# Optimization experiments

Measured on AMD Instinct MI355X. Metric: run time of the kernel, lower is better.

The kernel has to match this reference:

```python
import jax, jax.numpy as jnp
import numpy as np

B, T, I, H = 256, 2048, 64, 256


def setup_inputs() -> dict:
    key = jax.random.key(0)
    ks = jax.random.split(key, 8)
    s_ih = 1.0 / np.sqrt(H)
    return {
        "x": jax.random.normal(ks[0], (B, T, I), dtype=jnp.float32),
        "lengths": jax.random.randint(ks[1], (B,), 1, T + 1),  # in [1, T]
        "W_ih": jax.random.uniform(ks[2], (H, I), minval=-s_ih, maxval=s_ih),
        "W_hh": jax.random.uniform(ks[3], (H, H), minval=-s_ih, maxval=s_ih),
        "b_ih": jax.random.uniform(ks[4], (H,), minval=-s_ih, maxval=s_ih),
        "b_hh": jax.random.uniform(ks[5], (H,), minval=-s_ih, maxval=s_ih),
        "W_fc": jax.random.uniform(ks[6], (1, H), minval=-s_ih, maxval=s_ih),
        "b_fc": jax.random.uniform(ks[7], (1,), minval=-s_ih, maxval=s_ih),
    }


def reference(x, lengths, W_ih, W_hh, b_ih, b_hh, W_fc, b_fc):
    # Vanilla RNN (tanh), batch_first: h_t = tanh(x_t W_ih^T + b_ih + h_{t-1} W_hh^T + b_hh)
    batch = x.shape[0]
    h0 = jnp.zeros((batch, W_hh.shape[0]), dtype=x.dtype)
    # Precompute input projections for all timesteps in one big GEMM: [B, T, H]
    xp = jnp.einsum("bti,hi->bth", x, W_ih) + b_ih + b_hh

    def step(h, xt):  # xt: [B, H]
        h = jnp.tanh(xt + h @ W_hh.T)
        return h, h

    _, hs = jax.lax.scan(step, h0, jnp.swapaxes(xp, 0, 1))  # hs: [T, B, H]
    out = jnp.swapaxes(hs, 0, 1)  # [B, T, H]
    # Per-sample last valid timestep gather
    last = out[jnp.arange(batch), lengths - 1]  # [B, H]
    return last @ W_fc.T + b_fc  # [B, 1]
```

## Files before the change

kernel.cpp:

```cpp
#include <hip/hip_runtime.h>


static constexpr int nB = 256;
static constexpr int nT = 2048;
static constexpr int nI = 64;
static constexpr int nH = 256;
static constexpr int XBLK = 32;
static constexpr int THREADS = 512;

typedef _Float16 f16x8 __attribute__((ext_vector_type(8)));
typedef float f32x4 __attribute__((ext_vector_type(4)));

__device__ __forceinline__ float fast_tanh(float x) {
  float a = fabsf(x);
  float e = __expf(-2.0f * a);
  float r = (1.0f - e) / (1.0f + e);
  return copysignf(r, x);
}

__global__ __launch_bounds__(THREADS, 2)
void rnn_mfma(const float* __restrict__ x, const int* __restrict__ lengths,
              const float* __restrict__ Wih, const float* __restrict__ Whh,
              const float* __restrict__ bih, const float* __restrict__ bhh,
              const float* __restrict__ Wfc, const float* __restrict__ bfc,
              float* __restrict__ out)
{
  __shared__ __align__(16) _Float16 hbuf[2][nH];
  __shared__ __align__(16) _Float16 xbuf[2][XBLK * nI];
  __shared__ float red[THREADS / 64];

  const int b   = blockIdx.x;
  const int tid = threadIdx.x;
  const int w   = tid >> 6;
  const int l   = tid & 63;
  const int q   = l >> 4;
  const int n   = l & 15;
  const int len = lengths[b];
  const float* xb = x + (size_t)b * nT * nI;

  f16x8 Ah[2][8];
  f16x8 Ax[2][2];
#pragma unroll
  for (int mt = 0; mt < 2; ++mt) {
    const int row = 32 * w + 16 * mt + n;
#pragma unroll
    for (int kt = 0; kt < 8; ++kt) {
      const float* src = Whh + row * nH + 32 * kt + 8 * q;
      f16x8 a;
#pragma unroll
      for (int j = 0; j < 8; ++j) a[j] = (_Float16)src[j];
      Ah[mt][kt] = a;
    }
#pragma unroll
    for (int kt = 0; kt < 2; ++kt) {
      const float* src = Wih + row * nI + 32 * kt + 8 * q;
      f16x8 a;
#pragma unroll
      for (int j = 0; j < 8; ++j) a[j] = (_Float16)src[j];
      Ax[mt][kt] = a;
    }
  }
  f32x4 bias0, bias1;
#pragma unroll
  for (int r = 0; r < 4; ++r) {
    const int r0 = 32 * w + 4 * q + r;
    bias0[r] = bih[r0] + bhh[r0];
    bias1[r] = bih[r0 + 16] + bhh[r0 + 16];
  }
  const int mt_sel  = (n >> 2) & 1;
  const int reg_sel = n & 3;
  const int row_own = 32 * w + 16 * mt_sel + 4 * q + reg_sel;

  if (tid < nH) hbuf[0][tid] = (_Float16)0.f;
  {
    float4 v = *(const float4*)(xb + tid * 4);
    _Float16* d = xbuf[0] + tid * 4;
    d[0] = (_Float16)v.x; d[1] = (_Float16)v.y;
    d[2] = (_Float16)v.z; d[3] = (_Float16)v.w;
  }
  __syncthreads();

  int t = 0;
  for (int blk = 0; t < len; ++blk) {
    float4 pre;
    const bool havepre = ((blk + 1) * XBLK < len);
    if (havepre)
      pre = *(const float4*)(xb + (size_t)(blk + 1) * XBLK * nI + tid * 4);

    const int nsteps = min(XBLK, len - blk * XBLK);
    const _Float16* xB = xbuf[blk & 1];

    for (int s = 0; s < nsteps; ++s, ++t) {
      const _Float16* hsrc = hbuf[t & 1];
      const _Float16* xsrc = xB + s * nI;

      f32x4 acc0 = bias0, acc1 = bias1;
#pragma unroll
      for (int kt = 0; kt < 8; ++kt) {
        f16x8 Bh = *(const f16x8*)(hsrc + 32 * kt + 8 * q);
        acc0 = __builtin_amdgcn_mfma_f32_16x16x32_f16(Ah[0][kt], Bh, acc0, 0, 0, 0);
        acc1 = __builtin_amdgcn_mfma_f32_16x16x32_f16(Ah[1][kt], Bh, acc1, 0, 0, 0);
      }
#pragma unroll
      for (int kt = 0; kt < 2; ++kt) {
        f16x8 Bx = *(const f16x8*)(xsrc + 32 * kt + 8 * q);
        acc0 = __builtin_amdgcn_mfma_f32_16x16x32_f16(Ax[0][kt], Bx, acc0, 0, 0, 0);
        acc1 = __builtin_amdgcn_mfma_f32_16x16x32_f16(Ax[1][kt], Bx, acc1, 0, 0, 0);
      }

      f32x4 a = mt_sel ? acc1 : acc0;
      float lo = (reg_sel & 1) ? a[1] : a[0];
      float hi = (reg_sel & 1) ? a[3] : a[2];
      float v  = (reg_sel & 2) ? hi : lo;
      float hn = fast_tanh(v);

      if (s == nsteps - 1 && havepre) {
        _Float16* d = xbuf[(blk + 1) & 1] + tid * 4;
        d[0] = (_Float16)pre.x; d[1] = (_Float16)pre.y;
        d[2] = (_Float16)pre.z; d[3] = (_Float16)pre.w;
      }
      if (n < 8) hbuf[(t + 1) & 1][row_own] = (_Float16)hn;
      __syncthreads();
    }
  }

  float v = 0.f;
  if (tid < nH) v = (float)hbuf[len & 1][tid] * Wfc[tid];
#pragma unroll
  for (int off = 32; off; off >>= 1) v += __shfl_down(v, off);
  if (l == 0) red[w] = v;
  __syncthreads();
  if (tid == 0) {
    float acc = bfc[0];
#pragma unroll
    for (int i = 0; i < THREADS / 64; ++i) acc += red[i];
    out[b] = acc;
  }
}

extern "C" void kernel_launch(void* const* d_in, const int* in_sizes, int n_in,
                              void* d_out, int out_size, void* d_ws, size_t ws_size,
                              hipStream_t stream) {
  const float* x   = (const float*)d_in[0];
  const int* lens  = (const int*)d_in[1];
  const float* Wih = (const float*)d_in[2];
  const float* Whh = (const float*)d_in[3];
  const float* bih = (const float*)d_in[4];
  const float* bhh = (const float*)d_in[5];
  const float* Wfc = (const float*)d_in[6];
  const float* bfc = (const float*)d_in[7];
  float* out = (float*)d_out;

  rnn_mfma<<<nB, THREADS, 0, stream>>>(x, lens, Wih, Whh, bih, bhh, Wfc, bfc, out);
}
```

Before: 1.218 ms.

## Halve block to four waves, each computing four 16-row MFMA tiles per step

Cuts the block from 8 to 4 wavefronts, so each wave holds 64 rows of W_hh/W_ih in registers and issues four independent MFMA accumulation chains per step. This is meant to lower the cost of the per-timestep __syncthreads barrier and give each wave more independent MFMA work to hide latency. Every lane now writes one h element, and the x prefetch uses 8-wide f16 vector stores. In exchange, register pressure roughly doubles and the serial MFMA chain per wave gets longer, which may lengthen each step's critical path.

```diff
diff --git a/kernel.cpp b/kernel.cpp
--- a/kernel.cpp
+++ b/kernel.cpp
@@ -6,7 +6,7 @@
 static constexpr int nI = 64;
 static constexpr int nH = 256;
 static constexpr int XBLK = 32;
-static constexpr int THREADS = 512;
+static constexpr int THREADS = 256;
 
 typedef _Float16 f16x8 __attribute__((ext_vector_type(8)));
 typedef float f32x4 __attribute__((ext_vector_type(4)));
@@ -18,16 +18,16 @@
   return copysignf(r, x);
 }
 
-__global__ __launch_bounds__(THREADS, 2)
-void rnn_mfma(const float* __restrict__ x, const int* __restrict__ lengths,
-              const float* __restrict__ Wih, const float* __restrict__ Whh,
-              const float* __restrict__ bih, const float* __restrict__ bhh,
-              const float* __restrict__ Wfc, const float* __restrict__ bfc,
-              float* __restrict__ out)
+__global__ __launch_bounds__(THREADS, 1)
+void rnn_mfma4(const float* __restrict__ x, const int* __restrict__ lengths,
+               const float* __restrict__ Wih, const float* __restrict__ Whh,
+               const float* __restrict__ bih, const float* __restrict__ bhh,
+               const float* __restrict__ Wfc, const float* __restrict__ bfc,
+               float* __restrict__ out)
 {
   __shared__ __align__(16) _Float16 hbuf[2][nH];
   __shared__ __align__(16) _Float16 xbuf[2][XBLK * nI];
-  __shared__ float red[THREADS / 64];
+  __shared__ float red[4];
 
   const int b   = blockIdx.x;
   const int tid = threadIdx.x;
@@ -38,11 +38,11 @@
   const int len = lengths[b];
   const float* xb = x + (size_t)b * nT * nI;
 
-  f16x8 Ah[2][8];
-  f16x8 Ax[2][2];
+  f16x8 Ah[4][8];
+  f16x8 Ax[4][2];
 #pragma unroll
-  for (int mt = 0; mt < 2; ++mt) {
-    const int row = 32 * w + 16 * mt + n;
+  for (int mt = 0; mt < 4; ++mt) {
+    const int row = 64 * w + 16 * mt + n;
 #pragma unroll
     for (int kt = 0; kt < 8; ++kt) {
       const float* src = Whh + row * nH + 32 * kt + 8 * q;
@@ -60,32 +60,37 @@
       Ax[mt][kt] = a;
     }
   }
-  f32x4 bias0, bias1;
+  f32x4 bias[4];
 #pragma unroll
-  for (int r = 0; r < 4; ++r) {
-    const int r0 = 32 * w + 4 * q + r;
-    bias0[r] = bih[r0] + bhh[r0];
-    bias1[r] = bih[r0 + 16] + bhh[r0 + 16];
-  }
-  const int mt_sel  = (n >> 2) & 1;
+  for (int mt = 0; mt < 4; ++mt)
+#pragma unroll
+    for (int r = 0; r < 4; ++r) {
+      const int r0 = 64 * w + 16 * mt + 4 * q + r;
+      bias[mt][r] = bih[r0] + bhh[r0];
+    }
+  const int mt_sel  = n >> 2;
   const int reg_sel = n & 3;
-  const int row_own = 32 * w + 16 * mt_sel + 4 * q + reg_sel;
+  const int row_own = 64 * w + 16 * mt_sel + 4 * q + reg_sel;
 
-  if (tid < nH) hbuf[0][tid] = (_Float16)0.f;
+  hbuf[0][tid] = (_Float16)0.f;
   {
-    float4 v = *(const float4*)(xb + tid * 4);
-    _Float16* d = xbuf[0] + tid * 4;
-    d[0] = (_Float16)v.x; d[1] = (_Float16)v.y;
-    d[2] = (_Float16)v.z; d[3] = (_Float16)v.w;
+    float4 v0 = *(const float4*)(xb + tid * 8);
+    float4 v1 = *(const float4*)(xb + tid * 8 + 4);
+    f16x8 d = { (_Float16)v0.x, (_Float16)v0.y, (_Float16)v0.z, (_Float16)v0.w,
+                (_Float16)v1.x, (_Float16)v1.y, (_Float16)v1.z, (_Float16)v1.w };
+    *(f16x8*)(xbuf[0] + tid * 8) = d;
   }
   __syncthreads();
 
   int t = 0;
   for (int blk = 0; t < len; ++blk) {
-    float4 pre;
+    float4 pre0, pre1;
     const bool havepre = ((blk + 1) * XBLK < len);
-    if (havepre)
-      pre = *(const float4*)(xb + (size_t)(blk + 1) * XBLK * nI + tid * 4);
+    if (havepre) {
+      const float* ps = xb + (size_t)(blk + 1) * XBLK * nI + tid * 8;
+      pre0 = *(const float4*)ps;
+      pre1 = *(const float4*)(ps + 4);
+    }
 
     const int nsteps = min(XBLK, len - blk * XBLK);
     const _Float16* xB = xbuf[blk & 1];
@@ -94,48 +99,48 @@
       const _Float16* hsrc = hbuf[t & 1];
       const _Float16* xsrc = xB + s * nI;
 
-      f32x4 acc0 = bias0, acc1 = bias1;
+      f32x4 acc0 = bias[0], acc1 = bias[1], acc2 = bias[2], acc3 = bias[3];
 #pragma unroll
       for (int kt = 0; kt < 8; ++kt) {
         f16x8 Bh = *(const f16x8*)(hsrc + 32 * kt + 8 * q);
         acc0 = __builtin_amdgcn_mfma_f32_16x16x32_f16(Ah[0][kt], Bh, acc0, 0, 0, 0);
         acc1 = __builtin_amdgcn_mfma_f32_16x16x32_f16(Ah[1][kt], Bh, acc1, 0, 0, 0);
+        acc2 = __builtin_amdgcn_mfma_f32_16x16x32_f16(Ah[2][kt], Bh, acc2, 0, 0, 0);
+        acc3 = __builtin_amdgcn_mfma_f32_16x16x32_f16(Ah[3][kt], Bh, acc3, 0, 0, 0);
       }
 #pragma unroll
       for (int kt = 0; kt < 2; ++kt) {
         f16x8 Bx = *(const f16x8*)(xsrc + 32 * kt + 8 * q);
         acc0 = __builtin_amdgcn_mfma_f32_16x16x32_f16(Ax[0][kt], Bx, acc0, 0, 0, 0);
         acc1 = __builtin_amdgcn_mfma_f32_16x16x32_f16(Ax[1][kt], Bx, acc1, 0, 0, 0);
+        acc2 = __builtin_amdgcn_mfma_f32_16x16x32_f16(Ax[2][kt], Bx, acc2, 0, 0, 0);
+        acc3 = __builtin_amdgcn_mfma_f32_16x16x32_f16(Ax[3][kt], Bx, acc3, 0, 0, 0);
       }
 
-      f32x4 a = mt_sel ? acc1 : acc0;
+      f32x4 ax = (n & 4) ? acc1 : acc0;
+      f32x4 ay = (n & 4) ? acc3 : acc2;
+      f32x4 a  = (n & 8) ? ay : ax;
       float lo = (reg_sel & 1) ? a[1] : a[0];
       float hi = (reg_sel & 1) ? a[3] : a[2];
       float v  = (reg_sel & 2) ? hi : lo;
       float hn = fast_tanh(v);
 
       if (s == nsteps - 1 && havepre) {
-        _Float16* d = xbuf[(blk + 1) & 1] + tid * 4;
-        d[0] = (_Float16)pre.x; d[1] = (_Float16)pre.y;
-        d[2] = (_Float16)pre.z; d[3] = (_Float16)pre.w;
+        f16x8 d = { (_Float16)pre0.x, (_Float16)pre0.y, (_Float16)pre0.z, (_Float16)pre0.w,
+                    (_Float16)pre1.x, (_Float16)pre1.y, (_Float16)pre1.z, (_Float16)pre1.w };
+        *(f16x8*)(xbuf[(blk + 1) & 1] + tid * 8) = d;
       }
-      if (n < 8) hbuf[(t + 1) & 1][row_own] = (_Float16)hn;
+      hbuf[(t + 1) & 1][row_own] = (_Float16)hn;
       __syncthreads();
     }
   }
 
-  float v = 0.f;
-  if (tid < nH) v = (float)hbuf[len & 1][tid] * Wfc[tid];
+  float v = (float)hbuf[len & 1][tid] * Wfc[tid];
 #pragma unroll
   for (int off = 32; off; off >>= 1) v += __shfl_down(v, off);
   if (l == 0) red[w] = v;
   __syncthreads();
-  if (tid == 0) {
-    float acc = bfc[0];
-#pragma unroll
-    for (int i = 0; i < THREADS / 64; ++i) acc += red[i];
-    out[b] = acc;
-  }
+  if (tid == 0) out[b] = ((red[0] + red[1]) + (red[2] + red[3])) + bfc[0];
 }
 
 extern "C" void kernel_launch(void* const* d_in, const int* in_sizes, int n_in,
@@ -151,5 +156,5 @@
   const float* bfc = (const float*)d_in[7];
   float* out = (float*)d_out;
 
-  rnn_mfma<<<nB, THREADS, 0, stream>>>(x, lens, Wih, Whh, bih, bhh, Wfc, bfc, out);
+  rnn_mfma4<<<nB, THREADS, 0, stream>>>(x, lens, Wih, Whh, bih, bhh, Wfc, bfc, out);
 }
```

Measured after the change: 1.453 ms. 1.19x slower.

## Batch input projection per 16-step block off the recurrent critical path

Applied to the files above, without the earlier changes.

Instead of running 4 extra MFMAs for x_t·W_ih each timestep in the serial loop, the kernel computes the input projection plus bias for 16 timesteps at once with a batched MFMA (timesteps as M dimension), storing fp32 results in padded shared memory that is double buffered. Each step then starts its accumulators from a shared-memory load of the precomputed projection, which shortens the per-step dependency chain. The plain __syncthreads is also replaced by an inline-asm lgkmcnt wait plus s_barrier. In exchange, the block-boundary step now carries a burst of extra MFMAs and strided shared-memory stores, and the shared-memory footprint grows.

```diff
diff --git a/kernel.cpp b/kernel.cpp
--- a/kernel.cpp
+++ b/kernel.cpp
@@ -5,11 +5,16 @@
 static constexpr int nT = 2048;
 static constexpr int nI = 64;
 static constexpr int nH = 256;
-static constexpr int XBLK = 32;
+static constexpr int XPB = 16;
+static constexpr int XPS = nH + 4;
 static constexpr int THREADS = 512;
 
 typedef _Float16 f16x8 __attribute__((ext_vector_type(8)));
 typedef float f32x4 __attribute__((ext_vector_type(4)));
+
+__device__ __forceinline__ void barrier_lgkm() {
+  asm volatile("s_waitcnt lgkmcnt(0)\n\ts_barrier" ::: "memory");
+}
 
 __device__ __forceinline__ float fast_tanh(float x) {
   float a = fabsf(x);
@@ -19,15 +24,15 @@
 }
 
 __global__ __launch_bounds__(THREADS, 2)
-void rnn_mfma(const float* __restrict__ x, const int* __restrict__ lengths,
-              const float* __restrict__ Wih, const float* __restrict__ Whh,
-              const float* __restrict__ bih, const float* __restrict__ bhh,
-              const float* __restrict__ Wfc, const float* __restrict__ bfc,
-              float* __restrict__ out)
+void rnn_v4(const float* __restrict__ x, const int* __restrict__ lengths,
+            const float* __restrict__ Wih, const float* __restrict__ Whh,
+            const float* __restrict__ bih, const float* __restrict__ bhh,
+            const float* __restrict__ Wfc, const float* __restrict__ bfc,
+            float* __restrict__ out)
 {
   __shared__ __align__(16) _Float16 hbuf[2][nH];
-  __shared__ __align__(16) _Float16 xbuf[2][XBLK * nI];
-  __shared__ float red[THREADS / 64];
+  __shared__ __align__(16) float xpb[2][XPB * XPS];
+  __shared__ float red[8];
 
   const int b   = blockIdx.x;
   const int tid = threadIdx.x;
@@ -39,7 +44,6 @@
   const float* xb = x + (size_t)b * nT * nI;
 
   f16x8 Ah[2][8];
-  f16x8 Ax[2][2];
 #pragma unroll
   for (int mt = 0; mt < 2; ++mt) {
     const int row = 32 * w + 16 * mt + n;
@@ -51,61 +55,76 @@
       for (int j = 0; j < 8; ++j) a[j] = (_Float16)src[j];
       Ah[mt][kt] = a;
     }
+  }
+  f16x8 Bp[2][2];
+  float biasp[2];
+#pragma unroll
+  for (int ntl = 0; ntl < 2; ++ntl) {
+    const int hcol = 32 * w + 16 * ntl + n;
 #pragma unroll
     for (int kt = 0; kt < 2; ++kt) {
-      const float* src = Wih + row * nI + 32 * kt + 8 * q;
+      const float* src = Wih + hcol * nI + 32 * kt + 8 * q;
       f16x8 a;
 #pragma unroll
       for (int j = 0; j < 8; ++j) a[j] = (_Float16)src[j];
-      Ax[mt][kt] = a;
+      Bp[ntl][kt] = a;
     }
-  }
-  f32x4 bias0, bias1;
-#pragma unroll
-  for (int r = 0; r < 4; ++r) {
-    const int r0 = 32 * w + 4 * q + r;
-    bias0[r] = bih[r0] + bhh[r0];
-    bias1[r] = bih[r0 + 16] + bhh[r0 + 16];
+    biasp[ntl] = bih[hcol] + bhh[hcol];
   }
   const int mt_sel  = (n >> 2) & 1;
   const int reg_sel = n & 3;
   const int row_own = 32 * w + 16 * mt_sel + 4 * q + reg_sel;
 
+  {
+    const float* pr = xb + (size_t)n * nI + 8 * q;
+    float4 x0 = *(const float4*)(pr);
+    float4 x1 = *(const float4*)(pr + 4);
+    float4 x2 = *(const float4*)(pr + 32);
+    float4 x3 = *(const float4*)(pr + 36);
+    f16x8 A0 = { (_Float16)x0.x,(_Float16)x0.y,(_Float16)x0.z,(_Float16)x0.w,
+                 (_Float16)x1.x,(_Float16)x1.y,(_Float16)x1.z,(_Float16)x1.w };
+    f16x8 A1 = { (_Float16)x2.x,(_Float16)x2.y,(_Float16)x2.z,(_Float16)x2.w,
+                 (_Float16)x3.x,(_Float16)x3.y,(_Float16)x3.z,(_Float16)x3.w };
+#pragma unroll
+    for (int ntl = 0; ntl < 2; ++ntl) {
+      f32x4 c = { biasp[ntl], biasp[ntl], biasp[ntl], biasp[ntl] };
+      c = __builtin_amdgcn_mfma_f32_16x16x32_f16(A0, Bp[ntl][0], c, 0, 0, 0);
+      c = __builtin_amdgcn_mfma_f32_16x16x32_f16(A1, Bp[ntl][1], c, 0, 0, 0);
+      const int hc = 32 * w + 16 * ntl + n;
+#pragma unroll
+      for (int r = 0; r < 4; ++r) xpb[0][(4 * q + r) * XPS + hc] = c[r];
+    }
+  }
   if (tid < nH) hbuf[0][tid] = (_Float16)0.f;
-  {
-    float4 v = *(const float4*)(xb + tid * 4);
-    _Float16* d = xbuf[0] + tid * 4;
-    d[0] = (_Float16)v.x; d[1] = (_Float16)v.y;
-    d[2] = (_Float16)v.z; d[3] = (_Float16)v.w;
-  }
   __syncthreads();
 
   int t = 0;
   for (int blk = 0; t < len; ++blk) {
-    float4 pre;
-    const bool havepre = ((blk + 1) * XBLK < len);
-    if (havepre)
-      pre = *(const float4*)(xb + (size_t)(blk + 1) * XBLK * nI + tid * 4);
+    const int t0n = (blk + 1) * XPB;
+    const bool havenext = t0n < len;
+    float4 x0, x1, x2, x3;
+    if (havenext) {
+      const float* pr = xb + (size_t)(t0n + n) * nI + 8 * q;
+      x0 = *(const float4*)(pr);
+      x1 = *(const float4*)(pr + 4);
+      x2 = *(const float4*)(pr + 32);
+      x3 = *(const float4*)(pr + 36);
+    }
 
-    const int nsteps = min(XBLK, len - blk * XBLK);
-    const _Float16* xB = xbuf[blk & 1];
+    const int nsteps = min(XPB, len - blk * XPB);
+    const float* xpsrc = xpb[blk & 1];
 
     for (int s = 0; s < nsteps; ++s, ++t) {
       const _Float16* hsrc = hbuf[t & 1];
-      const _Float16* xsrc = xB + s * nI;
 
-      f32x4 acc0 = bias0, acc1 = bias1;
+      f32x4 acc0 = *(const f32x4*)(xpsrc + s * XPS + 32 * w + 4 * q);
+      f32x4 acc1 = *(const f32x4*)(xpsrc + s * XPS + 32 * w + 16 + 4 * q);
+
 #pragma unroll
       for (int kt = 0; kt < 8; ++kt) {
         f16x8 Bh = *(const f16x8*)(hsrc + 32 * kt + 8 * q);
         acc0 = __builtin_amdgcn_mfma_f32_16x16x32_f16(Ah[0][kt], Bh, acc0, 0, 0, 0);
         acc1 = __builtin_amdgcn_mfma_f32_16x16x32_f16(Ah[1][kt], Bh, acc1, 0, 0, 0);
-      }
-#pragma unroll
-      for (int kt = 0; kt < 2; ++kt) {
-        f16x8 Bx = *(const f16x8*)(xsrc + 32 * kt + 8 * q);
-        acc0 = __builtin_amdgcn_mfma_f32_16x16x32_f16(Ax[0][kt], Bx, acc0, 0, 0, 0);
-        acc1 = __builtin_amdgcn_mfma_f32_16x16x32_f16(Ax[1][kt], Bx, acc1, 0, 0, 0);
       }
 
       f32x4 a = mt_sel ? acc1 : acc0;
@@ -114,13 +133,25 @@
       float v  = (reg_sel & 2) ? hi : lo;
       float hn = fast_tanh(v);
 
-      if (s == nsteps - 1 && havepre) {
-        _Float16* d = xbuf[(blk + 1) & 1] + tid * 4;
-        d[0] = (_Float16)pre.x; d[1] = (_Float16)pre.y;
-        d[2] = (_Float16)pre.z; d[3] = (_Float16)pre.w;
+      if (s == nsteps - 1 && havenext) {
+        f16x8 A0 = { (_Float16)x0.x,(_Float16)x0.y,(_Float16)x0.z,(_Float16)x0.w,
+                     (_Float16)x1.x,(_Float16)x1.y,(_Float16)x1.z,(_Float16)x1.w };
+        f16x8 A1 = { (_Float16)x2.x,(_Float16)x2.y,(_Float16)x2.z,(_Float16)x2.w,
+                     (_Float16)x3.x,(_Float16)x3.y,(_Float16)x3.z,(_Float16)x3.w };
+        float* dst = xpb[(blk + 1) & 1];
+#pragma unroll
+        for (int ntl = 0; ntl < 2; ++ntl) {
+          f32x4 c = { biasp[ntl], biasp[ntl], biasp[ntl], biasp[ntl] };
+          c = __builtin_amdgcn_mfma_f32_16x16x32_f16(A0, Bp[ntl][0], c, 0, 0, 0);
+          c = __builtin_amdgcn_mfma_f32_16x16x32_f16(A1, Bp[ntl][1], c, 0, 0, 0);
+          const int hc = 32 * w + 16 * ntl + n;
+#pragma unroll
+          for (int r = 0; r < 4; ++r) dst[(4 * q + r) * XPS + hc] = c[r];
+        }
       }
+
       if (n < 8) hbuf[(t + 1) & 1][row_own] = (_Float16)hn;
-      __syncthreads();
+      barrier_lgkm();
     }
   }
 
@@ -133,7 +164,7 @@
   if (tid == 0) {
     float acc = bfc[0];
 #pragma unroll
-    for (int i = 0; i < THREADS / 64; ++i) acc += red[i];
+    for (int i = 0; i < 8; ++i) acc += red[i];
     out[b] = acc;
   }
 }
@@ -151,5 +182,5 @@
   const float* bfc = (const float*)d_in[7];
   float* out = (float*)d_out;
 
-  rnn_mfma<<<nB, THREADS, 0, stream>>>(x, lens, Wih, Whh, bih, bhh, Wfc, bfc, out);
+  rnn_v4<<<nB, THREADS, 0, stream>>>(x, lens, Wih, Whh, bih, bhh, Wfc, bfc, out);
 }
```

Measured after the change: 1.268 ms. 1.04x slower.
